# Performance work log

Measured on AMD Instinct MI355X. Metric: run time of the kernel, lower is better.

## Reference

```python
import jax, jax.numpy as jnp
import numpy as np

NUM_HEADS = 16
KERNEL_SIZE = 13


def setup_inputs() -> dict:
    key = jax.random.key(0)
    ks = jax.random.split(key, 6)
    B, L, C = 4, 4096, 512
    H, K = NUM_HEADS, KERNEL_SIZE
    x = jax.random.normal(ks[0], (B, L, C), dtype=jnp.float32)
    qkv_w = jax.random.normal(ks[1], (C, 3 * C), dtype=jnp.float32) * 0.02
    qkv_b = jnp.zeros((3 * C,), dtype=jnp.float32)
    rpb = jax.random.normal(ks[2], (H, 2 * K - 1), dtype=jnp.float32) * 0.02
    proj_w = jax.random.normal(ks[3], (C, C), dtype=jnp.float32) * 0.02
    proj_b = jnp.zeros((C,), dtype=jnp.float32)
    return {"x": x, "qkv_w": qkv_w, "qkv_b": qkv_b, "rpb": rpb,
            "proj_w": proj_w, "proj_b": proj_b}


def reference(x, qkv_w, qkv_b, rpb, proj_w, proj_b):
    B, L, C = x.shape
    H, K = NUM_HEADS, KERNEL_SIZE
    hd = C // H
    scale = hd ** -0.5
    kh = K // 2

    # qkv projection -> q,k,v each [B,H,L,hd]
    qkv = (x @ qkv_w + qkv_b).reshape(B, L, 3, H, hd).transpose(2, 0, 3, 1, 4)
    q, k, v = qkv[0] * scale, qkv[1], qkv[2]

    # NATTEN window: start index clamped so window stays in-bounds
    pos = jnp.arange(L)
    ni = jnp.clip(pos - kh, 0, L - K)              # [L] window start per query
    idx = ni[:, None] + jnp.arange(K)[None, :]     # [L,K] key positions
    # rpb index: (key_pos - query_pos) + (K-1)
    rpb_idx = (ni - pos + (K - 1))[:, None] + jnp.arange(K)[None, :]  # [L,K]

    k_win = k[:, :, idx, :]                        # [B,H,L,K,hd]
    v_win = v[:, :, idx, :]                        # [B,H,L,K,hd]

    attn = jnp.einsum('bhld,bhlkd->bhlk', q, k_win) + rpb[:, rpb_idx][None]
    attn = jax.nn.softmax(attn, axis=-1)

    out = jnp.einsum('bhlk,bhlkd->bhld', attn, v_win)  # [B,H,L,hd]
    out = out.transpose(0, 2, 1, 3).reshape(B, L, C)
    return out @ proj_w + proj_b
```

## Files before the change

kernel.cpp:

```cpp
#include <hip/hip_runtime.h>
#include <hip/hip_bf16.h>
#include <stdint.h>


typedef __attribute__((ext_vector_type(8))) short short8;
typedef __attribute__((ext_vector_type(4))) float f32x4;
typedef __attribute__((ext_vector_type(8))) unsigned short u16x8;
typedef __attribute__((ext_vector_type(4))) float float4v;

#define NB 4
#define NL 4096
#define NC 512
#define NH 16
#define HD 32
#define KW 13
#define KHALF 6
#define NM (NB*NL)

__device__ __forceinline__ float b2f(unsigned short u) {
  union { unsigned int i; float f; } x; x.i = ((unsigned int)u) << 16; return x.f;
}
__device__ __forceinline__ unsigned short f2b(float f) {
  __hip_bfloat16 h = __float2bfloat16(f);
  return __builtin_bit_cast(unsigned short, h);
}
__device__ __forceinline__ void gll16(const unsigned short* g, unsigned short* l) {
  __builtin_amdgcn_global_load_lds(
      (const __attribute__((address_space(1))) void*)g,
      (__attribute__((address_space(3))) void*)l, 16, 0, 0);
}

__global__ __launch_bounds__(256) void cvt_f32_bf16(const float* __restrict__ in,
                                                    unsigned short* __restrict__ out) {
  long i = (long)blockIdx.x * 256 + threadIdx.x;
  const float4v* in4 = (const float4v*)in;
  float4v a = in4[i * 2];
  float4v b = in4[i * 2 + 1];
  u16x8 u;
  u[0] = f2b(a.x); u[1] = f2b(a.y); u[2] = f2b(a.z); u[3] = f2b(a.w);
  u[4] = f2b(b.x); u[5] = f2b(b.y); u[6] = f2b(b.z); u[7] = f2b(b.w);
  ((u16x8*)out)[i] = u;
}

__global__ __launch_bounds__(256) void transpose_bf16(const float* __restrict__ in,
                                                      unsigned short* __restrict__ out,
                                                      int R, int C) {
  __shared__ float t[32][33];
  int c0 = blockIdx.x * 32;
  int r0 = blockIdx.y * 32;
  int tx = threadIdx.x;
  int ty = threadIdx.y;
  #pragma unroll
  for (int i = ty; i < 32; i += 8)
    t[i][tx] = in[(long)(r0 + i) * C + c0 + tx];
  __syncthreads();
  #pragma unroll
  for (int i = ty; i < 32; i += 8)
    out[(long)(c0 + i) * R + r0 + tx] = f2b(t[tx][i]);
}


__device__ __forceinline__ void stage_half(const unsigned short* __restrict__ G,
                                           long rowBase, int K, int kt,
                                           unsigned short* ldsDst, int tid) {
  int r  = tid >> 3;
  int ch = (tid & 7) ^ (r & 7);
  const unsigned short* s0 = G + (rowBase + r) * (long)K + kt * 64 + ch * 8;
  gll16(s0, ldsDst + tid * 8);
  gll16(s0 + 64 * (long)K, ldsDst + 4096 + tid * 8);
}

#define BAR() __builtin_amdgcn_s_barrier()
#define LGK0() asm volatile("s_waitcnt lgkmcnt(0)" ::: "memory")
#define VM(N) asm volatile("s_waitcnt vmcnt(" #N ")" ::: "memory")

#define DS_A(BUF, QM) do { \
  const char* _ba = (const char*)(lds + (BUF)*16384); \
  _Pragma("unroll") for (int ii = 0; ii < 2; ++ii) { \
    int _row = wm*64 + ((QM)*2+ii)*16 + lr; \
    _Pragma("unroll") for (int kb = 0; kb < 2; ++kb) \
      af[ii][kb] = *(const short8*)(_ba + _row*128 + (((kb*4+lk) ^ lr7) * 16)); \
  } \
} while (0)

#define DS_B(BUF, QN, BF) do { \
  const char* _bb = (const char*)(lds + 32768 + (BUF)*8192); \
  _Pragma("unroll") for (int jj = 0; jj < 2; ++jj) { \
    int _row = wn*64 + ((QN)*2+jj)*16 + lr; \
    _Pragma("unroll") for (int kb = 0; kb < 2; ++kb) \
      BF[jj][kb] = *(const short8*)(_bb + _row*128 + (((kb*4+lk) ^ lr7) * 16)); \
  } \
} while (0)

#define MMA(QM, QN, BF) do { \
  __builtin_amdgcn_s_setprio(1); \
  _Pragma("unroll") for (int ii = 0; ii < 2; ++ii) \
    _Pragma("unroll") for (int jj = 0; jj < 2; ++jj) \
      _Pragma("unroll") for (int kb = 0; kb < 2; ++kb) \
        acc[(QM)*2+ii][(QN)*2+jj] = __builtin_amdgcn_mfma_f32_16x16x32_bf16( \
            af[ii][kb], BF[jj][kb], acc[(QM)*2+ii][(QN)*2+jj], 0, 0, 0); \
  __builtin_amdgcn_s_setprio(0); \
} while (0)

template<int OUT_BF16>
__global__ __launch_bounds__(512, 2)
void gemm256(const unsigned short* __restrict__ A,
             const unsigned short* __restrict__ BT,
             const float* __restrict__ bias,
             void* __restrict__ Cout,
             int M, int N, int K, int tilesN) {
  __shared__ __align__(16) unsigned short lds[49152];

  int tid = threadIdx.x;
  int nwg = gridDim.x;
  int cpx = nwg >> 3;
  int wg  = ((int)blockIdx.x & 7) * cpx + ((int)blockIdx.x >> 3);
  int tm = wg / tilesN, tn = wg % tilesN;
  long mBase = (long)tm * 256;
  long nBase = (long)tn * 128;

  int lane = tid & 63, wave = tid >> 6;
  int wm = wave >> 1;
  int wn = wave & 1;
  int lr = lane & 15, lk = lane >> 4, lr7 = lr & 7;

  unsigned short* A0h0 = lds;
  unsigned short* A0h1 = lds + 8192;
  unsigned short* A1h0 = lds + 16384;
  unsigned short* A1h1 = lds + 16384 + 8192;
  unsigned short* B0   = lds + 32768;
  unsigned short* B1   = lds + 32768 + 8192;

  f32x4 acc[4][4];
  #pragma unroll
  for (int i = 0; i < 4; ++i)
    #pragma unroll
    for (int j = 0; j < 4; ++j) acc[i][j] = (f32x4){0.f, 0.f, 0.f, 0.f};

  short8 af[2][2], bf0[2][2], bf1[2][2];

  stage_half(BT, nBase,       K, 0, B0,   tid);
  stage_half(A,  mBase,       K, 0, A0h0, tid);
  stage_half(A,  mBase + 128, K, 0, A0h1, tid);
  stage_half(BT, nBase,       K, 1, B1,   tid);
  VM(2);
  BAR();

  #pragma unroll 1
  for (int it = 0; it < 4; ++it) {
    int kt = it * 2;
    bool s2 = (kt + 2) < 8;
    bool s3 = (kt + 3) < 8;

    DS_A(0, 0);
    DS_B(0, 0, bf0);
    DS_B(0, 1, bf1);
    stage_half(A, mBase,       K, kt + 1, A1h0, tid);
    stage_half(A, mBase + 128, K, kt + 1, A1h1, tid);
    BAR(); LGK0();
    MMA(0, 0, bf0);
    MMA(0, 1, bf1);
    BAR();
    DS_A(0, 1);
    if (s2) stage_half(BT, nBase, K, kt + 2, B0, tid);
    BAR(); LGK0();
    MMA(1, 1, bf1);
    MMA(1, 0, bf0);
    if (s2) { VM(2); } else { VM(0); }
    BAR();
    DS_A(1, 0);
    DS_B(1, 0, bf0);
    DS_B(1, 1, bf1);
    if (s2) {
      stage_half(A, mBase,       K, kt + 2, A0h0, tid);
      stage_half(A, mBase + 128, K, kt + 2, A0h1, tid);
    }
    BAR(); LGK0();
    MMA(0, 0, bf0);
    MMA(0, 1, bf1);
    BAR();
    DS_A(1, 1);
    if (s3) stage_half(BT, nBase, K, kt + 3, B1, tid);
    BAR(); LGK0();
    MMA(1, 1, bf1);
    MMA(1, 0, bf0);
    if (s2) VM(2);
    BAR();
  }

  long rowb = mBase + wm * 64 + (lane >> 4) * 4;
  int  colb = (int)nBase + wn * 64 + lr;
  if (OUT_BF16) {
    unsigned short* C = (unsigned short*)Cout;
    #pragma unroll
    for (int mi = 0; mi < 4; ++mi)
      #pragma unroll
      for (int nj = 0; nj < 4; ++nj) {
        int col = colb + nj * 16;
        float bv = bias[col];
        #pragma unroll
        for (int r = 0; r < 4; ++r)
          C[(rowb + mi * 16 + r) * (long)N + col] = f2b(acc[mi][nj][r] + bv);
      }
  } else {
    float* C = (float*)Cout;
    #pragma unroll
    for (int mi = 0; mi < 4; ++mi)
      #pragma unroll
      for (int nj = 0; nj < 4; ++nj) {
        int col = colb + nj * 16;
        float bv = bias[col];
        #pragma unroll
        for (int r = 0; r < 4; ++r)
          C[(rowb + mi * 16 + r) * (long)N + col] = acc[mi][nj][r] + bv;
      }
  }
}

__global__ __launch_bounds__(256)
void natt(const unsigned short* __restrict__ qkv, const float* __restrict__ rpb,
          unsigned short* __restrict__ out) {
  int tid = blockIdx.x * 256 + threadIdx.x;
  int h = tid & 15;
  int l = (tid >> 4) & (NL - 1);
  int b = tid >> 16;
  const float scale = 0.17677669529663687f;

  long qb = ((long)(b * NL + l) * 3) * NC + h * HD;
  float q[HD];
  {
    const u16x8* q8 = (const u16x8*)(qkv + qb);
    #pragma unroll
    for (int w = 0; w < 4; ++w) {
      u16x8 u = q8[w];
      #pragma unroll
      for (int e = 0; e < 8; ++e) q[w * 8 + e] = b2f(u[e]) * scale;
    }
  }

  int ni = l - KHALF;
  if (ni < 0) ni = 0;
  if (ni > NL - KW) ni = NL - KW;
  const float* rb = rpb + h * (2 * KW - 1) + (ni - l + KW - 1);

  float p[KW];
  float mx = -1e30f;
  #pragma unroll
  for (int j = 0; j < KW; ++j) {
    long kb = ((long)(b * NL + ni + j) * 3 + 1) * NC + h * HD;
    const u16x8* k8 = (const u16x8*)(qkv + kb);
    float s = 0.f;
    #pragma unroll
    for (int w = 0; w < 4; ++w) {
      u16x8 u = k8[w];
      #pragma unroll
      for (int e = 0; e < 8; ++e) s += q[w * 8 + e] * b2f(u[e]);
    }
    s += rb[j];
    p[j] = s;
    mx = fmaxf(mx, s);
  }

  float sum = 0.f;
  #pragma unroll
  for (int j = 0; j < KW; ++j) { p[j] = __expf(p[j] - mx); sum += p[j]; }
  float inv = 1.0f / sum;

  float o[HD];
  #pragma unroll
  for (int d = 0; d < HD; ++d) o[d] = 0.f;
  #pragma unroll
  for (int j = 0; j < KW; ++j) {
    long vb = ((long)(b * NL + ni + j) * 3 + 2) * NC + h * HD;
    const u16x8* v8 = (const u16x8*)(qkv + vb);
    float wj = p[j] * inv;
    #pragma unroll
    for (int w = 0; w < 4; ++w) {
      u16x8 u = v8[w];
      #pragma unroll
      for (int e = 0; e < 8; ++e) o[w * 8 + e] += wj * b2f(u[e]);
    }
  }

  unsigned short* op = out + (long)(b * NL + l) * NC + h * HD;
  #pragma unroll
  for (int w = 0; w < 4; ++w) {
    u16x8 u;
    #pragma unroll
    for (int e = 0; e < 8; ++e) u[e] = f2b(o[w * 8 + e]);
    *((u16x8*)(op + w * 8)) = u;
  }
}

extern "C" void kernel_launch(void* const* d_in, const int* in_sizes, int n_in,
                              void* d_out, int out_size, void* d_ws, size_t ws_size,
                              hipStream_t stream) {
  const float* x      = (const float*)d_in[0];
  const float* qkv_w  = (const float*)d_in[1];
  const float* qkv_b  = (const float*)d_in[2];
  const float* rpb    = (const float*)d_in[3];
  const float* proj_w = (const float*)d_in[4];
  const float* proj_b = (const float*)d_in[5];
  float* out = (float*)d_out;

  char* ws = (char*)d_ws;
  unsigned short* xb     = (unsigned short*)(ws);
  unsigned short* qkvwT  = (unsigned short*)(ws + 16777216);
  unsigned short* projwT = (unsigned short*)(ws + 18350080);
  unsigned short* qkvo   = (unsigned short*)(ws + 18874368);
  unsigned short* attno  = (unsigned short*)(ws + 69206016);

  cvt_f32_bf16<<<dim3(4096), dim3(256), 0, stream>>>(x, xb);
  transpose_bf16<<<dim3(48, 16), dim3(32, 8), 0, stream>>>(qkv_w, qkvwT, 512, 1536);
  transpose_bf16<<<dim3(16, 16), dim3(32, 8), 0, stream>>>(proj_w, projwT, 512, 512);
  gemm256<1><<<dim3(768), dim3(512), 0, stream>>>(xb, qkvwT, qkv_b, qkvo,
                                                  NM, 1536, 512, 12);
  natt<<<dim3(1024), dim3(256), 0, stream>>>(qkvo, rpb, attno);
  gemm256<0><<<dim3(256), dim3(512), 0, stream>>>(attno, projwT, proj_b, out,
                                                  NM, 512, 512, 4);
}
```

Measured before the change: 108.8 us.

## Triple-buffer GEMM LDS staging to prefetch two k-tiles ahead

```diff
diff --git a/kernel.cpp b/kernel.cpp
--- a/kernel.cpp
+++ b/kernel.cpp
@@ -74,8 +74,8 @@
 #define LGK0() asm volatile("s_waitcnt lgkmcnt(0)" ::: "memory")
 #define VM(N) asm volatile("s_waitcnt vmcnt(" #N ")" ::: "memory")
 
-#define DS_A(BUF, QM) do { \
-  const char* _ba = (const char*)(lds + (BUF)*16384); \
+#define DS_A(ABASE, QM) do { \
+  const char* _ba = (const char*)(ABASE); \
   _Pragma("unroll") for (int ii = 0; ii < 2; ++ii) { \
     int _row = wm*64 + ((QM)*2+ii)*16 + lr; \
     _Pragma("unroll") for (int kb = 0; kb < 2; ++kb) \
@@ -83,8 +83,8 @@
   } \
 } while (0)
 
-#define DS_B(BUF, QN, BF) do { \
-  const char* _bb = (const char*)(lds + 32768 + (BUF)*8192); \
+#define DS_B(BBASE, QN, BF) do { \
+  const char* _bb = (const char*)(BBASE); \
   _Pragma("unroll") for (int jj = 0; jj < 2; ++jj) { \
     int _row = wn*64 + ((QN)*2+jj)*16 + lr; \
     _Pragma("unroll") for (int kb = 0; kb < 2; ++kb) \
@@ -109,7 +109,7 @@
              const float* __restrict__ bias,
              void* __restrict__ Cout,
              int M, int N, int K, int tilesN) {
-  __shared__ __align__(16) unsigned short lds[49152];
+  __shared__ __align__(16) unsigned short lds[73728];
 
   int tid = threadIdx.x;
   int nwg = gridDim.x;
@@ -124,13 +124,6 @@
   int wn = wave & 1;
   int lr = lane & 15, lk = lane >> 4, lr7 = lr & 7;
 
-  unsigned short* A0h0 = lds;
-  unsigned short* A0h1 = lds + 8192;
-  unsigned short* A1h0 = lds + 16384;
-  unsigned short* A1h1 = lds + 16384 + 8192;
-  unsigned short* B0   = lds + 32768;
-  unsigned short* B1   = lds + 32768 + 8192;
-
   f32x4 acc[4][4];
   #pragma unroll
   for (int i = 0; i < 4; ++i)
@@ -139,53 +132,51 @@
 
   short8 af[2][2], bf0[2][2], bf1[2][2];
 
-  stage_half(BT, nBase,       K, 0, B0,   tid);
-  stage_half(A,  mBase,       K, 0, A0h0, tid);
-  stage_half(A,  mBase + 128, K, 0, A0h1, tid);
-  stage_half(BT, nBase,       K, 1, B1,   tid);
-  VM(2);
+  {
+    unsigned short* A0 = lds;
+    unsigned short* B0 = lds + 49152;
+    unsigned short* A1 = lds + 16384;
+    unsigned short* B1 = lds + 49152 + 8192;
+    stage_half(A,  mBase,       K, 0, A0,        tid);
+    stage_half(A,  mBase + 128, K, 0, A0 + 8192, tid);
+    stage_half(BT, nBase,       K, 0, B0,        tid);
+    stage_half(A,  mBase,       K, 1, A1,        tid);
+    stage_half(A,  mBase + 128, K, 1, A1 + 8192, tid);
+    stage_half(BT, nBase,       K, 1, B1,        tid);
+  }
+  VM(6);
   BAR();
 
+  int bc = 0;
   #pragma unroll 1
-  for (int it = 0; it < 4; ++it) {
-    int kt = it * 2;
-    bool s2 = (kt + 2) < 8;
-    bool s3 = (kt + 3) < 8;
-
-    DS_A(0, 0);
-    DS_B(0, 0, bf0);
-    DS_B(0, 1, bf1);
-    stage_half(A, mBase,       K, kt + 1, A1h0, tid);
-    stage_half(A, mBase + 128, K, kt + 1, A1h1, tid);
-    BAR(); LGK0();
-    MMA(0, 0, bf0);
-    MMA(0, 1, bf1);
-    BAR();
-    DS_A(0, 1);
-    if (s2) stage_half(BT, nBase, K, kt + 2, B0, tid);
-    BAR(); LGK0();
-    MMA(1, 1, bf1);
-    MMA(1, 0, bf0);
-    if (s2) { VM(2); } else { VM(0); }
-    BAR();
-    DS_A(1, 0);
-    DS_B(1, 0, bf0);
-    DS_B(1, 1, bf1);
-    if (s2) {
-      stage_half(A, mBase,       K, kt + 2, A0h0, tid);
-      stage_half(A, mBase + 128, K, kt + 2, A0h1, tid);
+  for (int kt = 0; kt < 8; ++kt) {
+    int bs = bc == 0 ? 2 : bc - 1;
+    unsigned short* A_cur = lds + bc * 16384;
+    unsigned short* B_cur = lds + 49152 + bc * 8192;
+    unsigned short* A_stg = lds + bs * 16384;
+    unsigned short* B_stg = lds + 49152 + bs * 8192;
+    bool st = (kt + 2) < 8;
+
+    DS_A(A_cur, 0);
+    DS_B(B_cur, 0, bf0);
+    DS_B(B_cur, 1, bf1);
+    if (st) {
+      stage_half(A, mBase,       K, kt + 2, A_stg,        tid);
+      stage_half(A, mBase + 128, K, kt + 2, A_stg + 8192, tid);
     }
     BAR(); LGK0();
     MMA(0, 0, bf0);
     MMA(0, 1, bf1);
     BAR();
-    DS_A(1, 1);
-    if (s3) stage_half(BT, nBase, K, kt + 3, B1, tid);
+    DS_A(A_cur, 1);
+    if (st) stage_half(BT, nBase, K, kt + 2, B_stg, tid);
     BAR(); LGK0();
     MMA(1, 1, bf1);
     MMA(1, 0, bf0);
-    if (s2) VM(2);
+    if (st)              VM(6);
+    else if (kt + 1 < 8) VM(0);
     BAR();
+    bc = bc == 2 ? 0 : bc + 1;
   }
 
   long rowb = mBase + wm * 64 + (lane >> 4) * 4;
```

Result: no change. 106.9 us (-1.7%).
